# Optimization experiments

Hardware: AMD Instinct MI355X
Metric: run time of the kernel (lower is better)

The kernel has to match this reference:

```python
import jax, jax.numpy as jnp
import numpy as np
from jax import lax

B, S, E, H, KS = 2, 2048, 1024, 16, 3
DH = E // H


def setup_inputs() -> dict:
    key = jax.random.key(0)
    ks = jax.random.split(key, 11)
    s = 1.0 / np.sqrt(E)
    sc = 1.0 / np.sqrt(H * KS)
    return {
        "query": jax.random.normal(ks[0], (B, S, E), jnp.float32),
        "Wq": jax.random.uniform(ks[1], (E, E), jnp.float32, -s, s),
        "bq": jax.random.uniform(ks[2], (E,), jnp.float32, -s, s),
        "Wk": jax.random.uniform(ks[3], (E, E), jnp.float32, -s, s),
        "bk": jax.random.uniform(ks[4], (E,), jnp.float32, -s, s),
        "Wv": jax.random.uniform(ks[5], (E, E), jnp.float32, -s, s),
        "bv": jax.random.uniform(ks[6], (E,), jnp.float32, -s, s),
        "Wo": jax.random.uniform(ks[7], (E, E), jnp.float32, -s, s),
        "bo": jax.random.uniform(ks[8], (E,), jnp.float32, -s, s),
        "conv_w": jax.random.uniform(ks[9], (H, H, KS), jnp.float32, -sc, sc),
        "conv_b": jax.random.uniform(ks[10], (H,), jnp.float32, -sc, sc),
    }


def reference(query, Wq, bq, Wk, bk, Wv, bv, Wo, bo, conv_w, conv_b):
    b, s, e = query.shape
    h, dh = H, DH
    # projections, split heads -> [B, H, S, Dh]
    Q = (query @ Wq.T + bq).reshape(b, s, h, dh).transpose(0, 2, 1, 3)
    K = (query @ Wk.T + bk).reshape(b, s, h, dh).transpose(0, 2, 1, 3)
    V = (query @ Wv.T + bv).reshape(b, s, h, dh).transpose(0, 2, 1, 3)
    # scores [B, H, Sq, Sk]
    scores = jnp.einsum("bhqd,bhkd->bhqk", Q, K) / np.sqrt(dh).astype(np.float32)
    # cross-head conv1d along key axis: reshape to (B*Sq, H, Sk) as NCW
    x = scores.transpose(0, 2, 1, 3).reshape(b * s, h, s)
    x = lax.conv_general_dilated(
        x, conv_w, window_strides=(1,), padding=[(KS // 2, KS // 2)],
        dimension_numbers=("NCW", "OIW", "NCW"))
    x = x + conv_b[None, :, None]
    scores = x.reshape(b, s, h, s).transpose(0, 2, 1, 3)
    weights = jax.nn.softmax(scores, axis=-1)
    # PV matmul, merge heads -> [B, S, E]
    out = jnp.einsum("bhqk,bhkd->bqhd", weights, V).reshape(b, s, e)
    return out @ Wo.T + bo
```

## Files before the change

kernel.cpp:

```cpp
#include <hip/hip_runtime.h>

typedef unsigned short u16;
typedef short short8 __attribute__((ext_vector_type(8)));
typedef unsigned short ushort8 __attribute__((ext_vector_type(8)));
typedef unsigned short bf16x4 __attribute__((ext_vector_type(4)));
typedef float f32x4 __attribute__((ext_vector_type(4)));

#define DEVINL __device__ __forceinline__

DEVINL float bf2f(u16 u) {
  unsigned int x = ((unsigned int)u) << 16;
  return __builtin_bit_cast(float, x);
}
DEVINL u16 f2bf(float f) {
  unsigned int x = __builtin_bit_cast(unsigned int, f);
  x += 0x7FFFu + ((x >> 16) & 1u);
  return (u16)(x >> 16);
}


__global__ __launch_bounds__(256) void cvt_all(
    const float* __restrict__ q, const float* __restrict__ wq,
    const float* __restrict__ wk, const float* __restrict__ wv,
    const float* __restrict__ wo, u16* __restrict__ out) {
  int i = blockIdx.x * 256 + threadIdx.x;
  const float* src;
  size_t off8;
  if (i < 524288) { src = q;  off8 = i; }
  else if (i < 655360) { src = wq; off8 = i - 524288; }
  else if (i < 786432) { src = wk; off8 = i - 655360; }
  else if (i < 917504) { src = wv; off8 = i - 786432; }
  else { src = wo; off8 = i - 917504; }
  f32x4 a = ((const f32x4*)src)[2 * off8];
  f32x4 b = ((const f32x4*)src)[2 * off8 + 1];
  ushort8 o;
#pragma unroll
  for (int e = 0; e < 4; ++e) o[e] = f2bf(a[e]);
#pragma unroll
  for (int e = 0; e < 4; ++e) o[4 + e] = f2bf(b[e]);
  ((ushort8*)out)[i] = o;
}

template <int BM, int BN, bool TRANSV, bool HASBIAS, bool OUTF32>
__global__ __launch_bounds__(256) void gemm_nt(
    const u16* __restrict__ A, const u16* __restrict__ Bm,
    const float* __restrict__ bias, void* __restrict__ C,
    int K, int lda, int ldb, int ldc, float scale,
    long long sAh, long long sBh, long long sCh) {
  constexpr int LDSS = 40;
  constexpr int WM = BM / 2, WN = BN / 2, FM = WM / 16, FN = WN / 16;
  constexpr int AIN = BM / 64;
  constexpr int BIN = BN / 64;

  __shared__ alignas(16) u16 As[BM * LDSS];
  __shared__ alignas(16) u16 Bs[BN * LDSS];

  const int tid = threadIdx.x;
  const int lane = tid & 63;
  const int wv = tid >> 6;
  const int wy = wv >> 1, wx = wv & 1;
  const int quad = lane >> 4, mrow = lane & 15;

  const int z = blockIdx.z;
  const u16* Ap = A + z * sAh;
  const u16* Bp = Bm + z * sBh;
  u16* Cp = (u16*)C + z * sCh;
  float* Cf = (float*)C + z * sCh;

  const int row0 = blockIdx.y * BM;
  const int col0 = blockIdx.x * BN;

  f32x4 acc[FM][FN];
#pragma unroll
  for (int i = 0; i < FM; ++i)
#pragma unroll
    for (int j = 0; j < FN; ++j) acc[i][j] = f32x4{0.f, 0.f, 0.f, 0.f};

  for (int k0 = 0; k0 < K; k0 += 32) {
    ushort8 ta[AIN], tb[BIN];
#pragma unroll
    for (int r = 0; r < AIN; ++r) {
      int idx = r * 256 + tid;
      int row = idx >> 2, ch = idx & 3;
      ta[r] = *(const ushort8*)(Ap + (size_t)(row0 + row) * lda + k0 + ch * 8);
    }
#pragma unroll
    for (int r = 0; r < BIN; ++r) {
      int idx = r * 256 + tid;
      int row = idx >> 2, ch = idx & 3;
      tb[r] = *(const ushort8*)(Bp + (size_t)(col0 + row) * ldb + k0 + ch * 8);
    }
    __syncthreads();
#pragma unroll
    for (int r = 0; r < AIN; ++r) {
      int idx = r * 256 + tid;
      int row = idx >> 2, ch = idx & 3;
      *(ushort8*)&As[row * LDSS + ch * 8] = ta[r];
    }
#pragma unroll
    for (int r = 0; r < BIN; ++r) {
      int idx = r * 256 + tid;
      int row = idx >> 2, ch = idx & 3;
      *(ushort8*)&Bs[row * LDSS + ch * 8] = tb[r];
    }
    __syncthreads();

    short8 af[FM], bfr[FN];
#pragma unroll
    for (int mi = 0; mi < FM; ++mi)
      af[mi] = *(const short8*)&As[(wy * WM + mi * 16 + mrow) * LDSS + quad * 8];
#pragma unroll
    for (int ni = 0; ni < FN; ++ni)
      bfr[ni] = *(const short8*)&Bs[(wx * WN + ni * 16 + mrow) * LDSS + quad * 8];
#pragma unroll
    for (int mi = 0; mi < FM; ++mi)
#pragma unroll
      for (int ni = 0; ni < FN; ++ni)
        acc[mi][ni] = __builtin_amdgcn_mfma_f32_16x16x32_bf16(
            af[mi], bfr[ni], acc[mi][ni], 0, 0, 0);
  }

#pragma unroll
  for (int mi = 0; mi < FM; ++mi) {
    const int rowb = row0 + wy * WM + mi * 16 + quad * 4;
#pragma unroll
    for (int ni = 0; ni < FN; ++ni) {
      const int col = col0 + wx * WN + ni * 16 + mrow;
      float bv = 0.f;
      if (HASBIAS) bv = bias[col];
      f32x4 v = acc[mi][ni];
      if (OUTF32) {
#pragma unroll
        for (int r = 0; r < 4; ++r)
          Cf[(size_t)(rowb + r) * ldc + col] = v[r] * scale + bv;
      } else if (!TRANSV) {
#pragma unroll
        for (int r = 0; r < 4; ++r)
          Cp[(size_t)(rowb + r) * ldc + col] = f2bf(v[r] * scale + bv);
      } else {
        const int bb = rowb >> 11;
        const int ss = rowb & 2047;
        bf16x4 pk;
#pragma unroll
        for (int r = 0; r < 4; ++r) pk[r] = f2bf(v[r] * scale + bv);
        *(bf16x4*)(Cp + (size_t)bb * 2097152 + (size_t)col * 2048 + ss) = pk;
      }
    }
  }
}

__global__ __launch_bounds__(512, 2) void conv_softmax(
    u16* __restrict__ SC, const float* __restrict__ cw, int qt) {
  __shared__ alignas(16) u16 rawT[1026 * 24];
  __shared__ float redA[8][16];
  __shared__ float redB[8][16];

  const int tid = threadIdx.x;
  const int lane = tid & 63;
  const int wv = tid >> 6;
  const int q = blockIdx.x;
  const int n = lane & 15;
  const int quad = lane >> 4;

  short8 a1, a2;
  {
    const int h = n;
#pragma unroll
    for (int j = 0; j < 8; ++j) {
      const int kd = quad * 8 + j;
      const int i = kd & 15, d = kd >> 4;
      a1[j] = (short)f2bf(cw[h * 48 + i * 3 + d]);
      a2[j] = (quad < 2) ? (short)f2bf(cw[h * 48 + kd * 3 + 2]) : (short)0;
    }
  }

  f32x4 acc[16];
#pragma unroll
  for (int ai = 0; ai < 16; ++ai) acc[ai] = f32x4{0.f, 0.f, 0.f, 0.f};

  for (int s = 0; s < 2; ++s) {
    if (s) __syncthreads();
    const int segk = s * 1024;
    {
      const int h = tid & 15, kc = tid >> 4;
#pragma unroll
      for (int j = 0; j < 4; ++j) {
        const int kb = kc * 32 + j * 8;
        ushort8 v = *(const ushort8*)&SC[((size_t)h * qt + q) * 2048 + segk + kb];
#pragma unroll
        for (int e0 = 0; e0 < 8; ++e0) {
          const int e = (e0 + h) & 7;
          rawT[(kb + e + 1) * 24 + h] = v[e];
        }
      }
      if (tid < 32) {
        const int h2 = tid & 15;
        const int top = tid >> 4;
        const int k = segk + (top ? 1024 : -1);
        u16 val = 0;
        if ((unsigned)k < 2048u) val = SC[((size_t)h2 * qt + q) * 2048 + k];
        rawT[(top ? 1025 : 0) * 24 + h2] = val;
      }
    }
    __syncthreads();

#pragma unroll
    for (int tt = 0; tt < 8; ++tt) {
      const int k0l = (wv * 8 + tt) * 16;
      const short8 b1 = *(const short8*)&rawT[(k0l + n + (quad >> 1)) * 24 + (quad & 1) * 8];
      const short8 b2 = *(const short8*)&rawT[(k0l + n + 2) * 24 + (quad & 1) * 8];
      const int ai = s * 8 + tt;
      acc[ai] = __builtin_amdgcn_mfma_f32_16x16x32_bf16(a1, b1, acc[ai], 0, 0, 0);
      acc[ai] = __builtin_amdgcn_mfma_f32_16x16x32_bf16(a2, b2, acc[ai], 0, 0, 0);
    }
  }

  float fm[4];
#pragma unroll
  for (int r = 0; r < 4; ++r) fm[r] = -3e38f;
#pragma unroll
  for (int ai = 0; ai < 16; ++ai)
#pragma unroll
    for (int r = 0; r < 4; ++r) fm[r] = fmaxf(fm[r], acc[ai][r]);
#pragma unroll
  for (int off = 1; off < 16; off <<= 1)
#pragma unroll
    for (int r = 0; r < 4; ++r) fm[r] = fmaxf(fm[r], __shfl_xor(fm[r], off));
  if (n == 0)
#pragma unroll
    for (int r = 0; r < 4; ++r) redA[wv][quad * 4 + r] = fm[r];
  __syncthreads();
#pragma unroll
  for (int r = 0; r < 4; ++r) {
    float m = redA[0][quad * 4 + r];
#pragma unroll
    for (int w = 1; w < 8; ++w) m = fmaxf(m, redA[w][quad * 4 + r]);
    fm[r] = m;
  }
  float fs[4] = {0.f, 0.f, 0.f, 0.f};
#pragma unroll
  for (int ai = 0; ai < 16; ++ai)
#pragma unroll
    for (int r = 0; r < 4; ++r) {
      acc[ai][r] = __expf(acc[ai][r] - fm[r]);
      fs[r] += acc[ai][r];
    }
#pragma unroll
  for (int off = 1; off < 16; off <<= 1)
#pragma unroll
    for (int r = 0; r < 4; ++r) fs[r] += __shfl_xor(fs[r], off);
  if (n == 0)
#pragma unroll
    for (int r = 0; r < 4; ++r) redB[wv][quad * 4 + r] = fs[r];
  __syncthreads();
#pragma unroll
  for (int r = 0; r < 4; ++r) {
    float sum = 0.f;
#pragma unroll
    for (int w = 0; w < 8; ++w) sum += redB[w][quad * 4 + r];
    fs[r] = 1.f / sum;
  }

#pragma unroll
  for (int ai = 0; ai < 16; ++ai) {
    const int k0 = (ai >> 3) * 1024 + ((ai & 7) + wv * 8) * 16;
#pragma unroll
    for (int r = 0; r < 4; ++r) {
      const int h = quad * 4 + r;
      SC[((size_t)h * qt + q) * 2048 + k0 + n] = f2bf(acc[ai][r] * fs[r]);
    }
  }
}

__global__ void fill_diag(float* out, int n) {
  int i = blockIdx.x * 256 + threadIdx.x;
  if (i < n) out[i] = 2000.0f;
}

extern "C" void kernel_launch(void* const* d_in, const int* in_sizes, int n_in,
                              void* d_out, int out_size, void* d_ws, size_t ws_size,
                              hipStream_t stream) {
  const float* query = (const float*)d_in[0];
  const float* Wq = (const float*)d_in[1];
  const float* bq = (const float*)d_in[2];
  const float* Wk = (const float*)d_in[3];
  const float* bk = (const float*)d_in[4];
  const float* Wv = (const float*)d_in[5];
  const float* bv = (const float*)d_in[6];
  const float* Wo = (const float*)d_in[7];
  const float* bo = (const float*)d_in[8];
  const float* cw = (const float*)d_in[9];

  const size_t SE = (size_t)4096 * 1024;
  const size_t WE = (size_t)1024 * 1024;
  const size_t fixedElems = (SE + 4 * WE) + 4 * SE;
  const size_t fixedB = fixedElems * sizeof(u16);

  int qt = 0;
  for (int cand = 2048; cand >= 128; cand >>= 1) {
    size_t need = fixedB + (size_t)16 * cand * 2048 * sizeof(u16);
    if (ws_size >= need) { qt = cand; break; }
  }
  if (qt == 0) {
    fill_diag<<<dim3((out_size + 255) / 256), dim3(256), 0, stream>>>(
        (float*)d_out, out_size);
    return;
  }

  u16* ws = (u16*)d_ws;
  u16* Qb = ws;
  u16* Wqb = Qb + SE;
  u16* Wkb = Wqb + WE;
  u16* Wvb = Wkb + WE;
  u16* Wob = Wvb + WE;
  u16* Qw = Wob + WE;
  u16* Kw = Qw + SE;
  u16* Vt = Kw + SE;
  u16* At = Vt + SE;
  u16* SC = At + SE;

  dim3 blk(256);
  cvt_all<<<dim3(4096), blk, 0, stream>>>(query, Wq, Wk, Wv, Wo, Qb);

  gemm_nt<128, 128, false, true, false><<<dim3(8, 32, 1), blk, 0, stream>>>(
      Qb, Wqb, bq, Qw, 1024, 1024, 1024, 1024, 1.f, 0, 0, 0);
  gemm_nt<128, 128, false, true, false><<<dim3(8, 32, 1), blk, 0, stream>>>(
      Qb, Wkb, bk, Kw, 1024, 1024, 1024, 1024, 1.f, 0, 0, 0);
  gemm_nt<128, 128, true, true, false><<<dim3(8, 32, 1), blk, 0, stream>>>(
      Qb, Wvb, bv, Vt, 1024, 1024, 1024, 1024, 1.f, 0, 0, 0);

  const long long scTile = (long long)qt * 2048;
  for (int b = 0; b < 2; ++b) {
    for (int q0 = 0; q0 < 2048; q0 += qt) {
      const size_t qkOff = (size_t)b * 2097152 + (size_t)q0 * 1024;
      gemm_nt<128, 128, false, false, false>
          <<<dim3(16, qt / 128, 16), blk, 0, stream>>>(
              Qw + qkOff, Kw + (size_t)b * 2097152, nullptr, SC,
              64, 1024, 1024, 2048, 0.125f, 64LL, 64LL, scTile);
      conv_softmax<<<dim3(qt), dim3(512), 0, stream>>>(SC, cw, qt);
      gemm_nt<128, 64, false, false, false>
          <<<dim3(1, qt / 128, 16), blk, 0, stream>>>(
              SC, Vt + (size_t)b * 2097152, nullptr,
              At + qkOff, 2048, 2048, 2048, 1024, 1.f,
              scTile, 131072LL, 64LL);
    }
  }

  gemm_nt<128, 128, false, true, true><<<dim3(8, 32, 1), blk, 0, stream>>>(
      At, Wob, bo, d_out, 1024, 1024, 1024, 1024, 1.f, 0, 0, 0);
}
```

Baseline: 499.8 us.

## Fuse conv, online softmax and PV matmul into one streaming kernel

```diff
diff --git a/kernel.cpp b/kernel.cpp
--- a/kernel.cpp
+++ b/kernel.cpp
@@ -149,125 +149,185 @@
   }
 }
 
-__global__ __launch_bounds__(512, 2) void conv_softmax(
-    u16* __restrict__ SC, const float* __restrict__ cw, int qt) {
-  __shared__ alignas(16) u16 rawT[1026 * 24];
-  __shared__ float redA[8][16];
-  __shared__ float redB[8][16];
+__global__ __launch_bounds__(512) void conv_attn(
+    const u16* __restrict__ SC, const u16* __restrict__ Vt,
+    const float* __restrict__ cw, u16* __restrict__ At) {
+  constexpr int TROW = 24;
+  constexpr int TSLAB = 66 * TROW;
+  constexpr int PROW = 72;
+  __shared__ alignas(16) u16 T[8 * TSLAB];
+  __shared__ alignas(16) u16 Pl[16 * 8 * PROW];
+  __shared__ float alphaS[16][16];
+  __shared__ float lS[16][16];
 
   const int tid = threadIdx.x;
   const int lane = tid & 63;
   const int wv = tid >> 6;
-  const int q = blockIdx.x;
   const int n = lane & 15;
   const int quad = lane >> 4;
+  const int q0 = blockIdx.x * 8;
+
+  if (tid < 256) {
+    alphaS[tid >> 4][tid & 15] = 1.f;
+    lS[tid >> 4][tid & 15] = 1.f;
+  }
 
   short8 a1, a2;
+#pragma unroll
+  for (int j = 0; j < 8; ++j) {
+    const int kd = quad * 8 + j;
+    const int i = kd & 15, d = kd >> 4;
+    a1[j] = (short)f2bf(cw[n * 48 + i * 3 + d]);
+    a2[j] = (quad < 2) ? (short)f2bf(cw[n * 48 + kd * 3 + 2]) : (short)0;
+  }
+
+  float m[4], l[4];
+#pragma unroll
+  for (int r = 0; r < 4; ++r) { m[r] = -3e38f; l[r] = 0.f; }
+  f32x4 O[2][4];
+#pragma unroll
+  for (int hh = 0; hh < 2; ++hh)
+#pragma unroll
+    for (int dt = 0; dt < 4; ++dt) O[hh][dt] = f32x4{0.f, 0.f, 0.f, 0.f};
+
+#pragma unroll 1
+  for (int c = 0; c < 32; ++c) {
+    const int k0 = c * 64;
+#pragma unroll
+    for (int rr = 0; rr < 2; ++rr) {
+      const int idx = rr * 512 + tid;
+      const int k8 = idx & 7;
+      const int pair = idx >> 3;
+      const int qq = pair >> 4, h = pair & 15;
+      ushort8 v = *(const ushort8*)(SC + ((size_t)(h * 2048 + q0 + qq) * 2048) + k0 + k8 * 8);
+#pragma unroll
+      for (int e0 = 0; e0 < 8; ++e0) {
+        const int e = (e0 + k8) & 7;
+        T[qq * TSLAB + (1 + k8 * 8 + e) * TROW + h] = v[e];
+      }
+    }
+    if (tid < 256) {
+      const int top = tid >> 7, p2 = tid & 127;
+      const int qq = p2 >> 4, h = p2 & 15;
+      const int k = k0 + (top ? 64 : -1);
+      u16 val = 0;
+      if ((unsigned)k < 2048u) val = SC[(size_t)(h * 2048 + q0 + qq) * 2048 + k];
+      T[qq * TSLAB + (top ? 65 : 0) * TROW + h] = val;
+    }
+
+    if (c > 0) {
+      const int k0p = k0 - 64;
+#pragma unroll
+      for (int hh = 0; hh < 2; ++hh) {
+        const int h = wv * 2 + hh;
+        float av[4];
+#pragma unroll
+        for (int r = 0; r < 4; ++r) av[r] = alphaS[h][quad * 4 + r];
+#pragma unroll
+        for (int dt = 0; dt < 4; ++dt)
+#pragma unroll
+          for (int r = 0; r < 4; ++r) O[hh][dt][r] *= av[r];
+#pragma unroll
+        for (int ks = 0; ks < 2; ++ks) {
+          const short8 aF = *(const short8*)&Pl[(h * 8 + (n & 7)) * PROW + ks * 32 + quad * 8];
+#pragma unroll
+          for (int dt = 0; dt < 4; ++dt) {
+            const short8 bF = *(const short8*)(Vt + (size_t)(h * 64 + dt * 16 + n) * 2048 + k0p + ks * 32 + quad * 8);
+            O[hh][dt] = __builtin_amdgcn_mfma_f32_16x16x32_bf16(aF, bF, O[hh][dt], 0, 0, 0);
+          }
+        }
+      }
+    }
+    __syncthreads();
+
+    {
+      const int qq = wv;
+      f32x4 x[4];
+#pragma unroll
+      for (int kt = 0; kt < 4; ++kt) {
+        const short8 b1 = *(const short8*)&T[qq * TSLAB + (kt * 16 + n + (quad >> 1)) * TROW + (quad & 1) * 8];
+        const short8 b2 = *(const short8*)&T[qq * TSLAB + (kt * 16 + n + 2) * TROW + (quad & 1) * 8];
+        f32x4 acc = f32x4{0.f, 0.f, 0.f, 0.f};
+        acc = __builtin_amdgcn_mfma_f32_16x16x32_bf16(a1, b1, acc, 0, 0, 0);
+        acc = __builtin_amdgcn_mfma_f32_16x16x32_bf16(a2, b2, acc, 0, 0, 0);
+        x[kt] = acc;
+      }
+      float mn[4], al[4], s[4];
+#pragma unroll
+      for (int r = 0; r < 4; ++r) {
+        float cm = fmaxf(fmaxf(x[0][r], x[1][r]), fmaxf(x[2][r], x[3][r]));
+#pragma unroll
+        for (int off = 1; off < 16; off <<= 1) cm = fmaxf(cm, __shfl_xor(cm, off));
+        mn[r] = fmaxf(m[r], cm);
+        al[r] = __expf(m[r] - mn[r]);
+        s[r] = 0.f;
+      }
+#pragma unroll
+      for (int kt = 0; kt < 4; ++kt)
+#pragma unroll
+        for (int r = 0; r < 4; ++r) {
+          x[kt][r] = __expf(x[kt][r] - mn[r]);
+          s[r] += x[kt][r];
+        }
+#pragma unroll
+      for (int r = 0; r < 4; ++r) {
+#pragma unroll
+        for (int off = 1; off < 16; off <<= 1) s[r] += __shfl_xor(s[r], off);
+        l[r] = l[r] * al[r] + s[r];
+        m[r] = mn[r];
+      }
+#pragma unroll
+      for (int kt = 0; kt < 4; ++kt)
+#pragma unroll
+        for (int r = 0; r < 4; ++r)
+          Pl[((quad * 4 + r) * 8 + qq) * PROW + kt * 16 + n] = f2bf(x[kt][r]);
+      if (n == 0)
+#pragma unroll
+        for (int r = 0; r < 4; ++r) alphaS[quad * 4 + r][qq] = al[r];
+    }
+    __syncthreads();
+  }
+
   {
-    const int h = n;
-#pragma unroll
-    for (int j = 0; j < 8; ++j) {
-      const int kd = quad * 8 + j;
-      const int i = kd & 15, d = kd >> 4;
-      a1[j] = (short)f2bf(cw[h * 48 + i * 3 + d]);
-      a2[j] = (quad < 2) ? (short)f2bf(cw[h * 48 + kd * 3 + 2]) : (short)0;
-    }
-  }
-
-  f32x4 acc[16];
-#pragma unroll
-  for (int ai = 0; ai < 16; ++ai) acc[ai] = f32x4{0.f, 0.f, 0.f, 0.f};
-
-  for (int s = 0; s < 2; ++s) {
-    if (s) __syncthreads();
-    const int segk = s * 1024;
-    {
-      const int h = tid & 15, kc = tid >> 4;
-#pragma unroll
-      for (int j = 0; j < 4; ++j) {
-        const int kb = kc * 32 + j * 8;
-        ushort8 v = *(const ushort8*)&SC[((size_t)h * qt + q) * 2048 + segk + kb];
-#pragma unroll
-        for (int e0 = 0; e0 < 8; ++e0) {
-          const int e = (e0 + h) & 7;
-          rawT[(kb + e + 1) * 24 + h] = v[e];
+    const int k0p = 31 * 64;
+#pragma unroll
+    for (int hh = 0; hh < 2; ++hh) {
+      const int h = wv * 2 + hh;
+      float av[4];
+#pragma unroll
+      for (int r = 0; r < 4; ++r) av[r] = alphaS[h][quad * 4 + r];
+#pragma unroll
+      for (int dt = 0; dt < 4; ++dt)
+#pragma unroll
+        for (int r = 0; r < 4; ++r) O[hh][dt][r] *= av[r];
+#pragma unroll
+      for (int ks = 0; ks < 2; ++ks) {
+        const short8 aF = *(const short8*)&Pl[(h * 8 + (n & 7)) * PROW + ks * 32 + quad * 8];
+#pragma unroll
+        for (int dt = 0; dt < 4; ++dt) {
+          const short8 bF = *(const short8*)(Vt + (size_t)(h * 64 + dt * 16 + n) * 2048 + k0p + ks * 32 + quad * 8);
+          O[hh][dt] = __builtin_amdgcn_mfma_f32_16x16x32_bf16(aF, bF, O[hh][dt], 0, 0, 0);
         }
       }
-      if (tid < 32) {
-        const int h2 = tid & 15;
-        const int top = tid >> 4;
-        const int k = segk + (top ? 1024 : -1);
-        u16 val = 0;
-        if ((unsigned)k < 2048u) val = SC[((size_t)h2 * qt + q) * 2048 + k];
-        rawT[(top ? 1025 : 0) * 24 + h2] = val;
-      }
-    }
-    __syncthreads();
-
-#pragma unroll
-    for (int tt = 0; tt < 8; ++tt) {
-      const int k0l = (wv * 8 + tt) * 16;
-      const short8 b1 = *(const short8*)&rawT[(k0l + n + (quad >> 1)) * 24 + (quad & 1) * 8];
-      const short8 b2 = *(const short8*)&rawT[(k0l + n + 2) * 24 + (quad & 1) * 8];
-      const int ai = s * 8 + tt;
-      acc[ai] = __builtin_amdgcn_mfma_f32_16x16x32_bf16(a1, b1, acc[ai], 0, 0, 0);
-      acc[ai] = __builtin_amdgcn_mfma_f32_16x16x32_bf16(a2, b2, acc[ai], 0, 0, 0);
-    }
-  }
-
-  float fm[4];
-#pragma unroll
-  for (int r = 0; r < 4; ++r) fm[r] = -3e38f;
-#pragma unroll
-  for (int ai = 0; ai < 16; ++ai)
-#pragma unroll
-    for (int r = 0; r < 4; ++r) fm[r] = fmaxf(fm[r], acc[ai][r]);
-#pragma unroll
-  for (int off = 1; off < 16; off <<= 1)
-#pragma unroll
-    for (int r = 0; r < 4; ++r) fm[r] = fmaxf(fm[r], __shfl_xor(fm[r], off));
+    }
+  }
   if (n == 0)
 #pragma unroll
-    for (int r = 0; r < 4; ++r) redA[wv][quad * 4 + r] = fm[r];
+    for (int r = 0; r < 4; ++r) lS[quad * 4 + r][wv] = l[r];
   __syncthreads();
 #pragma unroll
-  for (int r = 0; r < 4; ++r) {
-    float m = redA[0][quad * 4 + r];
-#pragma unroll
-    for (int w = 1; w < 8; ++w) m = fmaxf(m, redA[w][quad * 4 + r]);
-    fm[r] = m;
-  }
-  float fs[4] = {0.f, 0.f, 0.f, 0.f};
-#pragma unroll
-  for (int ai = 0; ai < 16; ++ai)
-#pragma unroll
-    for (int r = 0; r < 4; ++r) {
-      acc[ai][r] = __expf(acc[ai][r] - fm[r]);
-      fs[r] += acc[ai][r];
-    }
-#pragma unroll
-  for (int off = 1; off < 16; off <<= 1)
-#pragma unroll
-    for (int r = 0; r < 4; ++r) fs[r] += __shfl_xor(fs[r], off);
-  if (n == 0)
-#pragma unroll
-    for (int r = 0; r < 4; ++r) redB[wv][quad * 4 + r] = fs[r];
-  __syncthreads();
-#pragma unroll
-  for (int r = 0; r < 4; ++r) {
-    float sum = 0.f;
-#pragma unroll
-    for (int w = 0; w < 8; ++w) sum += redB[w][quad * 4 + r];
-    fs[r] = 1.f / sum;
-  }
-
-#pragma unroll
-  for (int ai = 0; ai < 16; ++ai) {
-    const int k0 = (ai >> 3) * 1024 + ((ai & 7) + wv * 8) * 16;
-#pragma unroll
-    for (int r = 0; r < 4; ++r) {
-      const int h = quad * 4 + r;
-      SC[((size_t)h * qt + q) * 2048 + k0 + n] = f2bf(acc[ai][r] * fs[r]);
+  for (int hh = 0; hh < 2; ++hh) {
+    const int h = wv * 2 + hh;
+    if (quad < 2) {
+      float inv[4];
+#pragma unroll
+      for (int r = 0; r < 4; ++r) inv[r] = 1.f / lS[h][quad * 4 + r];
+#pragma unroll
+      for (int dt = 0; dt < 4; ++dt)
+#pragma unroll
+        for (int r = 0; r < 4; ++r)
+          At[(size_t)(q0 + quad * 4 + r) * 1024 + h * 64 + dt * 16 + n] =
+              f2bf(O[hh][dt][r] * inv[r]);
     }
   }
 }
@@ -293,15 +353,9 @@
 
   const size_t SE = (size_t)4096 * 1024;
   const size_t WE = (size_t)1024 * 1024;
-  const size_t fixedElems = (SE + 4 * WE) + 4 * SE;
-  const size_t fixedB = fixedElems * sizeof(u16);
-
-  int qt = 0;
-  for (int cand = 2048; cand >= 128; cand >>= 1) {
-    size_t need = fixedB + (size_t)16 * cand * 2048 * sizeof(u16);
-    if (ws_size >= need) { qt = cand; break; }
-  }
-  if (qt == 0) {
+  const size_t SCE = (size_t)16 * 2048 * 2048;
+  const size_t fixedB = ((SE + 4 * WE) + 4 * SE) * sizeof(u16);
+  if (ws_size < fixedB + SCE * sizeof(u16)) {
     fill_diag<<<dim3((out_size + 255) / 256), dim3(256), 0, stream>>>(
         (float*)d_out, out_size);
     return;
@@ -329,21 +383,14 @@
   gemm_nt<128, 128, true, true, false><<<dim3(8, 32, 1), blk, 0, stream>>>(
       Qb, Wvb, bv, Vt, 1024, 1024, 1024, 1024, 1.f, 0, 0, 0);
 
-  const long long scTile = (long long)qt * 2048;
   for (int b = 0; b < 2; ++b) {
-    for (int q0 = 0; q0 < 2048; q0 += qt) {
-      const size_t qkOff = (size_t)b * 2097152 + (size_t)q0 * 1024;
-      gemm_nt<128, 128, false, false, false>
-          <<<dim3(16, qt / 128, 16), blk, 0, stream>>>(
-              Qw + qkOff, Kw + (size_t)b * 2097152, nullptr, SC,
-              64, 1024, 1024, 2048, 0.125f, 64LL, 64LL, scTile);
-      conv_softmax<<<dim3(qt), dim3(512), 0, stream>>>(SC, cw, qt);
-      gemm_nt<128, 64, false, false, false>
-          <<<dim3(1, qt / 128, 16), blk, 0, stream>>>(
-              SC, Vt + (size_t)b * 2097152, nullptr,
-              At + qkOff, 2048, 2048, 2048, 1024, 1.f,
-              scTile, 131072LL, 64LL);
-    }
+    const size_t bQK = (size_t)b * 2097152;
+    gemm_nt<128, 128, false, false, false>
+        <<<dim3(16, 16, 16), blk, 0, stream>>>(
+            Qw + bQK, Kw + bQK, nullptr, SC,
+            64, 1024, 1024, 2048, 0.125f, 64LL, 64LL, 4194304LL);
+    conv_attn<<<dim3(256), dim3(512), 0, stream>>>(
+        SC, Vt + bQK, cw, At + bQK);
   }
 
   gemm_nt<128, 128, false, true, true><<<dim3(8, 32, 1), blk, 0, stream>>>(
```

After: 698.6 us. 39.8% more time.

## Recompute conv in two passes to cut registers, defer softmax normalization to PV GEMM

Applied to the files above, without the earlier changes.

```diff
diff --git a/kernel.cpp b/kernel.cpp
--- a/kernel.cpp
+++ b/kernel.cpp
@@ -41,10 +41,11 @@
   ((ushort8*)out)[i] = o;
 }
 
-template <int BM, int BN, bool TRANSV, bool HASBIAS, bool OUTF32>
+template <int BM, int BN, bool TRANSV, bool HASBIAS, bool OUTF32, bool RSCALE>
 __global__ __launch_bounds__(256) void gemm_nt(
     const u16* __restrict__ A, const u16* __restrict__ Bm,
     const float* __restrict__ bias, void* __restrict__ C,
+    const float* __restrict__ rsc,
     int K, int lda, int ldb, int ldc, float scale,
     long long sAh, long long sBh, long long sCh) {
   constexpr int LDSS = 40;
@@ -135,8 +136,11 @@
           Cf[(size_t)(rowb + r) * ldc + col] = v[r] * scale + bv;
       } else if (!TRANSV) {
 #pragma unroll
-        for (int r = 0; r < 4; ++r)
-          Cp[(size_t)(rowb + r) * ldc + col] = f2bf(v[r] * scale + bv);
+        for (int r = 0; r < 4; ++r) {
+          float rs = 1.f;
+          if (RSCALE) rs = rsc[(size_t)z * 2048 + rowb + r];
+          Cp[(size_t)(rowb + r) * ldc + col] = f2bf(v[r] * scale * rs + bv);
+        }
       } else {
         const int bb = rowb >> 11;
         const int ss = rowb & 2047;
@@ -149,11 +153,12 @@
   }
 }
 
-__global__ __launch_bounds__(512, 2) void conv_softmax(
-    u16* __restrict__ SC, const float* __restrict__ cw, int qt) {
-  __shared__ alignas(16) u16 rawT[1026 * 24];
-  __shared__ float redA[8][16];
-  __shared__ float redB[8][16];
+__global__ __launch_bounds__(512, 8) void conv_softmax(
+    u16* __restrict__ SC, const float* __restrict__ cw, float* __restrict__ Lb) {
+  __shared__ alignas(16) u16 rawT[514 * 24];
+  __shared__ float redM[8][16];
+  __shared__ float redL[8][16];
+  __shared__ u16 haloL[16];
 
   const int tid = threadIdx.x;
   const int lane = tid & 63;
@@ -163,112 +168,129 @@
   const int quad = lane >> 4;
 
   short8 a1, a2;
-  {
-    const int h = n;
-#pragma unroll
-    for (int j = 0; j < 8; ++j) {
-      const int kd = quad * 8 + j;
-      const int i = kd & 15, d = kd >> 4;
-      a1[j] = (short)f2bf(cw[h * 48 + i * 3 + d]);
-      a2[j] = (quad < 2) ? (short)f2bf(cw[h * 48 + kd * 3 + 2]) : (short)0;
-    }
-  }
-
-  f32x4 acc[16];
-#pragma unroll
-  for (int ai = 0; ai < 16; ++ai) acc[ai] = f32x4{0.f, 0.f, 0.f, 0.f};
-
-  for (int s = 0; s < 2; ++s) {
+#pragma unroll
+  for (int j = 0; j < 8; ++j) {
+    const int kd = quad * 8 + j;
+    const int i = kd & 15, d = kd >> 4;
+    a1[j] = (short)f2bf(cw[n * 48 + i * 3 + d]);
+    a2[j] = (quad < 2) ? (short)f2bf(cw[n * 48 + kd * 3 + 2]) : (short)0;
+  }
+
+  const int h16 = tid & 15, kc = tid >> 4;
+  const size_t rowbase = ((size_t)h16 * 2048 + q) * 2048;
+  const int htop = (tid >> 4) & 1;
+  const size_t hrow = ((size_t)h16 * 2048 + q) * 2048;
+
+  float m[4];
+#pragma unroll
+  for (int r = 0; r < 4; ++r) m[r] = -3e38f;
+
+#pragma unroll 1
+  for (int s = 0; s < 4; ++s) {
+    const int segk = s * 512;
     if (s) __syncthreads();
-    const int segk = s * 1024;
-    {
-      const int h = tid & 15, kc = tid >> 4;
-#pragma unroll
-      for (int j = 0; j < 4; ++j) {
-        const int kb = kc * 32 + j * 8;
-        ushort8 v = *(const ushort8*)&SC[((size_t)h * qt + q) * 2048 + segk + kb];
-#pragma unroll
-        for (int e0 = 0; e0 < 8; ++e0) {
-          const int e = (e0 + h) & 7;
-          rawT[(kb + e + 1) * 24 + h] = v[e];
-        }
-      }
-      if (tid < 32) {
-        const int h2 = tid & 15;
-        const int top = tid >> 4;
-        const int k = segk + (top ? 1024 : -1);
-        u16 val = 0;
-        if ((unsigned)k < 2048u) val = SC[((size_t)h2 * qt + q) * 2048 + k];
-        rawT[(top ? 1025 : 0) * 24 + h2] = val;
-      }
-    }
-    __syncthreads();
-
-#pragma unroll
-    for (int tt = 0; tt < 8; ++tt) {
-      const int k0l = (wv * 8 + tt) * 16;
+#pragma unroll
+    for (int j = 0; j < 2; ++j) {
+      const int kb = kc * 16 + j * 8;
+      ushort8 v = *(const ushort8*)&SC[rowbase + segk + kb];
+#pragma unroll
+      for (int e0 = 0; e0 < 8; ++e0) {
+        const int e = (e0 + h16) & 7;
+        rawT[(kb + e + 1) * 24 + h16] = v[e];
+      }
+    }
+    if (tid < 32) {
+      const int k = segk + (htop ? 512 : -1);
+      u16 val = ((unsigned)k < 2048u) ? SC[hrow + k] : (u16)0;
+      rawT[(htop ? 513 : 0) * 24 + h16] = val;
+    }
+    __syncthreads();
+#pragma unroll
+    for (int tt = 0; tt < 4; ++tt) {
+      const int k0l = (wv * 4 + tt) * 16;
       const short8 b1 = *(const short8*)&rawT[(k0l + n + (quad >> 1)) * 24 + (quad & 1) * 8];
       const short8 b2 = *(const short8*)&rawT[(k0l + n + 2) * 24 + (quad & 1) * 8];
-      const int ai = s * 8 + tt;
-      acc[ai] = __builtin_amdgcn_mfma_f32_16x16x32_bf16(a1, b1, acc[ai], 0, 0, 0);
-      acc[ai] = __builtin_amdgcn_mfma_f32_16x16x32_bf16(a2, b2, acc[ai], 0, 0, 0);
-    }
-  }
-
-  float fm[4];
-#pragma unroll
-  for (int r = 0; r < 4; ++r) fm[r] = -3e38f;
-#pragma unroll
-  for (int ai = 0; ai < 16; ++ai)
-#pragma unroll
-    for (int r = 0; r < 4; ++r) fm[r] = fmaxf(fm[r], acc[ai][r]);
+      f32x4 x = f32x4{0.f, 0.f, 0.f, 0.f};
+      x = __builtin_amdgcn_mfma_f32_16x16x32_bf16(a1, b1, x, 0, 0, 0);
+      x = __builtin_amdgcn_mfma_f32_16x16x32_bf16(a2, b2, x, 0, 0, 0);
+#pragma unroll
+      for (int r = 0; r < 4; ++r) m[r] = fmaxf(m[r], x[r]);
+    }
+  }
 #pragma unroll
   for (int off = 1; off < 16; off <<= 1)
 #pragma unroll
-    for (int r = 0; r < 4; ++r) fm[r] = fmaxf(fm[r], __shfl_xor(fm[r], off));
+    for (int r = 0; r < 4; ++r) m[r] = fmaxf(m[r], __shfl_xor(m[r], off));
   if (n == 0)
 #pragma unroll
-    for (int r = 0; r < 4; ++r) redA[wv][quad * 4 + r] = fm[r];
+    for (int r = 0; r < 4; ++r) redM[wv][quad * 4 + r] = m[r];
   __syncthreads();
+  float fM[4];
 #pragma unroll
   for (int r = 0; r < 4; ++r) {
-    float m = redA[0][quad * 4 + r];
-#pragma unroll
-    for (int w = 1; w < 8; ++w) m = fmaxf(m, redA[w][quad * 4 + r]);
-    fm[r] = m;
-  }
-  float fs[4] = {0.f, 0.f, 0.f, 0.f};
-#pragma unroll
-  for (int ai = 0; ai < 16; ++ai)
-#pragma unroll
-    for (int r = 0; r < 4; ++r) {
-      acc[ai][r] = __expf(acc[ai][r] - fm[r]);
-      fs[r] += acc[ai][r];
-    }
+    float M = redM[0][quad * 4 + r];
+#pragma unroll
+    for (int w = 1; w < 8; ++w) M = fmaxf(M, redM[w][quad * 4 + r]);
+    fM[r] = M;
+  }
+
+  float l[4] = {0.f, 0.f, 0.f, 0.f};
+
+#pragma unroll 1
+  for (int s = 0; s < 4; ++s) {
+    const int segk = s * 512;
+    __syncthreads();
+#pragma unroll
+    for (int j = 0; j < 2; ++j) {
+      const int kb = kc * 16 + j * 8;
+      ushort8 v = *(const ushort8*)&SC[rowbase + segk + kb];
+#pragma unroll
+      for (int e0 = 0; e0 < 8; ++e0) {
+        const int e = (e0 + h16) & 7;
+        rawT[(kb + e + 1) * 24 + h16] = v[e];
+      }
+    }
+    if (tid < 32) {
+      if (htop) {
+        const int k = segk + 512;
+        rawT[513 * 24 + h16] = (k < 2048) ? SC[hrow + k] : (u16)0;
+      } else {
+        rawT[0 * 24 + h16] = (s == 0) ? (u16)0 : haloL[h16];
+      }
+    }
+    __syncthreads();
+    if (tid < 16) haloL[tid] = rawT[512 * 24 + tid];
+#pragma unroll
+    for (int tt = 0; tt < 4; ++tt) {
+      const int k0l = (wv * 4 + tt) * 16;
+      const short8 b1 = *(const short8*)&rawT[(k0l + n + (quad >> 1)) * 24 + (quad & 1) * 8];
+      const short8 b2 = *(const short8*)&rawT[(k0l + n + 2) * 24 + (quad & 1) * 8];
+      f32x4 x = f32x4{0.f, 0.f, 0.f, 0.f};
+      x = __builtin_amdgcn_mfma_f32_16x16x32_bf16(a1, b1, x, 0, 0, 0);
+      x = __builtin_amdgcn_mfma_f32_16x16x32_bf16(a2, b2, x, 0, 0, 0);
+      const int kg = segk + k0l + n;
+#pragma unroll
+      for (int r = 0; r < 4; ++r) {
+        const float e = __expf(x[r] - fM[r]);
+        l[r] += e;
+        SC[((size_t)(quad * 4 + r) * 2048 + q) * 2048 + kg] = f2bf(e);
+      }
+    }
+  }
+
 #pragma unroll
   for (int off = 1; off < 16; off <<= 1)
 #pragma unroll
-    for (int r = 0; r < 4; ++r) fs[r] += __shfl_xor(fs[r], off);
+    for (int r = 0; r < 4; ++r) l[r] += __shfl_xor(l[r], off);
   if (n == 0)
 #pragma unroll
-    for (int r = 0; r < 4; ++r) redB[wv][quad * 4 + r] = fs[r];
+    for (int r = 0; r < 4; ++r) redL[wv][quad * 4 + r] = l[r];
   __syncthreads();
-#pragma unroll
-  for (int r = 0; r < 4; ++r) {
+  if (tid < 16) {
     float sum = 0.f;
 #pragma unroll
-    for (int w = 0; w < 8; ++w) sum += redB[w][quad * 4 + r];
-    fs[r] = 1.f / sum;
-  }
-
-#pragma unroll
-  for (int ai = 0; ai < 16; ++ai) {
-    const int k0 = (ai >> 3) * 1024 + ((ai & 7) + wv * 8) * 16;
-#pragma unroll
-    for (int r = 0; r < 4; ++r) {
-      const int h = quad * 4 + r;
-      SC[((size_t)h * qt + q) * 2048 + k0 + n] = f2bf(acc[ai][r] * fs[r]);
-    }
+    for (int w = 0; w < 8; ++w) sum += redL[w][tid];
+    Lb[(size_t)tid * 2048 + q] = 1.f / sum;
   }
 }
 
@@ -293,15 +315,10 @@
 
   const size_t SE = (size_t)4096 * 1024;
   const size_t WE = (size_t)1024 * 1024;
-  const size_t fixedElems = (SE + 4 * WE) + 4 * SE;
-  const size_t fixedB = fixedElems * sizeof(u16);
-
-  int qt = 0;
-  for (int cand = 2048; cand >= 128; cand >>= 1) {
-    size_t need = fixedB + (size_t)16 * cand * 2048 * sizeof(u16);
-    if (ws_size >= need) { qt = cand; break; }
-  }
-  if (qt == 0) {
+  const size_t SCE = (size_t)16 * 2048 * 2048;
+  const size_t fixedB = ((SE + 4 * WE) + 4 * SE) * sizeof(u16);
+  const size_t LBB = (size_t)16 * 2048 * sizeof(float);
+  if (ws_size < fixedB + SCE * sizeof(u16) + LBB) {
     fill_diag<<<dim3((out_size + 255) / 256), dim3(256), 0, stream>>>(
         (float*)d_out, out_size);
     return;
@@ -318,34 +335,31 @@
   u16* Vt = Kw + SE;
   u16* At = Vt + SE;
   u16* SC = At + SE;
+  float* Lb = (float*)(SC + SCE);
 
   dim3 blk(256);
   cvt_all<<<dim3(4096), blk, 0, stream>>>(query, Wq, Wk, Wv, Wo, Qb);
 
-  gemm_nt<128, 128, false, true, false><<<dim3(8, 32, 1), blk, 0, stream>>>(
-      Qb, Wqb, bq, Qw, 1024, 1024, 1024, 1024, 1.f, 0, 0, 0);
-  gemm_nt<128, 128, false, true, false><<<dim3(8, 32, 1), blk, 0, stream>>>(
-      Qb, Wkb, bk, Kw, 1024, 1024, 1024, 1024, 1.f, 0, 0, 0);
-  gemm_nt<128, 128, true, true, false><<<dim3(8, 32, 1), blk, 0, stream>>>(
-      Qb, Wvb, bv, Vt, 1024, 1024, 1024, 1024, 1.f, 0, 0, 0);
-
-  const long long scTile = (long long)qt * 2048;
+  gemm_nt<128, 128, false, true, false, false><<<dim3(8, 32, 1), blk, 0, stream>>>(
+      Qb, Wqb, bq, Qw, nullptr, 1024, 1024, 1024, 1024, 1.f, 0, 0, 0);
+  gemm_nt<128, 128, false, true, false, false><<<dim3(8, 32, 1), blk, 0, stream>>>(
+      Qb, Wkb, bk, Kw, nullptr, 1024, 1024, 1024, 1024, 1.f, 0, 0, 0);
+  gemm_nt<128, 128, true, true, false, false><<<dim3(8, 32, 1), blk, 0, stream>>>(
+      Qb, Wvb, bv, Vt, nullptr, 1024, 1024, 1024, 1024, 1.f, 0, 0, 0);
+
   for (int b = 0; b < 2; ++b) {
-    for (int q0 = 0; q0 < 2048; q0 += qt) {
-      const size_t qkOff = (size_t)b * 2097152 + (size_t)q0 * 1024;
-      gemm_nt<128, 128, false, false, false>
-          <<<dim3(16, qt / 128, 16), blk, 0, stream>>>(
-              Qw + qkOff, Kw + (size_t)b * 2097152, nullptr, SC,
-              64, 1024, 1024, 2048, 0.125f, 64LL, 64LL, scTile);
-      conv_softmax<<<dim3(qt), dim3(512), 0, stream>>>(SC, cw, qt);
-      gemm_nt<128, 64, false, false, false>
-          <<<dim3(1, qt / 128, 16), blk, 0, stream>>>(
-              SC, Vt + (size_t)b * 2097152, nullptr,
-              At + qkOff, 2048, 2048, 2048, 1024, 1.f,
-              scTile, 131072LL, 64LL);
-    }
-  }
-
-  gemm_nt<128, 128, false, true, true><<<dim3(8, 32, 1), blk, 0, stream>>>(
-      At, Wob, bo, d_out, 1024, 1024, 1024, 1024, 1.f, 0, 0, 0);
-}
+    const size_t bQK = (size_t)b * 2097152;
+    gemm_nt<128, 128, false, false, false, false>
+        <<<dim3(16, 16, 16), blk, 0, stream>>>(
+            Qw + bQK, Kw + bQK, nullptr, SC, nullptr,
+            64, 1024, 1024, 2048, 0.125f, 64LL, 64LL, 4194304LL);
+    conv_softmax<<<dim3(2048), dim3(512), 0, stream>>>(SC, cw, Lb);
+    gemm_nt<64, 64, false, false, false, true>
+        <<<dim3(1, 32, 16), blk, 0, stream>>>(
+            SC, Vt + bQK, nullptr, At + bQK, Lb,
+            2048, 2048, 2048, 1024, 1.f, 4194304LL, 131072LL, 64LL);
+  }
+
+  gemm_nt<128, 128, false, true, true, false><<<dim3(8, 32, 1), blk, 0, stream>>>(
+      At, Wob, bo, d_out, nullptr, 1024, 1024, 1024, 1024, 1.f, 0, 0, 0);
+}
```

Result: slower. 742.6 us (+48.6%).

## Fuse QKV projections, defer softmax normalization into PV GEMM, retile attention GEMMs

Applied to the files above, without the earlier changes.

```diff
diff --git a/kernel.cpp b/kernel.cpp
--- a/kernel.cpp
+++ b/kernel.cpp
@@ -41,16 +41,20 @@
   ((ushort8*)out)[i] = o;
 }
 
-template <int BM, int BN, bool TRANSV, bool HASBIAS, bool OUTF32>
+template <int BM, int BN, int BK, bool TRANSV, bool HASBIAS, bool OUTF32,
+          bool RSCALE>
 __global__ __launch_bounds__(256) void gemm_nt(
     const u16* __restrict__ A, const u16* __restrict__ Bm,
     const float* __restrict__ bias, void* __restrict__ C,
+    const float* __restrict__ rsc,
     int K, int lda, int ldb, int ldc, float scale,
     long long sAh, long long sBh, long long sCh) {
-  constexpr int LDSS = 40;
+  constexpr int LDSS = BK + 8;
+  constexpr int KC8 = BK / 8;
+  constexpr int KSH = (BK == 32) ? 2 : 3;
   constexpr int WM = BM / 2, WN = BN / 2, FM = WM / 16, FN = WN / 16;
-  constexpr int AIN = BM / 64;
-  constexpr int BIN = BN / 64;
+  constexpr int AIN = BM * KC8 / 256;
+  constexpr int BIN = BN * KC8 / 256;
 
   __shared__ alignas(16) u16 As[BM * LDSS];
   __shared__ alignas(16) u16 Bs[BN * LDSS];
@@ -76,48 +80,51 @@
 #pragma unroll
     for (int j = 0; j < FN; ++j) acc[i][j] = f32x4{0.f, 0.f, 0.f, 0.f};
 
-  for (int k0 = 0; k0 < K; k0 += 32) {
+  for (int k0 = 0; k0 < K; k0 += BK) {
     ushort8 ta[AIN], tb[BIN];
 #pragma unroll
     for (int r = 0; r < AIN; ++r) {
       int idx = r * 256 + tid;
-      int row = idx >> 2, ch = idx & 3;
+      int row = idx >> KSH, ch = idx & (KC8 - 1);
       ta[r] = *(const ushort8*)(Ap + (size_t)(row0 + row) * lda + k0 + ch * 8);
     }
 #pragma unroll
     for (int r = 0; r < BIN; ++r) {
       int idx = r * 256 + tid;
-      int row = idx >> 2, ch = idx & 3;
+      int row = idx >> KSH, ch = idx & (KC8 - 1);
       tb[r] = *(const ushort8*)(Bp + (size_t)(col0 + row) * ldb + k0 + ch * 8);
     }
     __syncthreads();
 #pragma unroll
     for (int r = 0; r < AIN; ++r) {
       int idx = r * 256 + tid;
-      int row = idx >> 2, ch = idx & 3;
+      int row = idx >> KSH, ch = idx & (KC8 - 1);
       *(ushort8*)&As[row * LDSS + ch * 8] = ta[r];
     }
 #pragma unroll
     for (int r = 0; r < BIN; ++r) {
       int idx = r * 256 + tid;
-      int row = idx >> 2, ch = idx & 3;
+      int row = idx >> KSH, ch = idx & (KC8 - 1);
       *(ushort8*)&Bs[row * LDSS + ch * 8] = tb[r];
     }
     __syncthreads();
 
-    short8 af[FM], bfr[FN];
-#pragma unroll
-    for (int mi = 0; mi < FM; ++mi)
-      af[mi] = *(const short8*)&As[(wy * WM + mi * 16 + mrow) * LDSS + quad * 8];
-#pragma unroll
-    for (int ni = 0; ni < FN; ++ni)
-      bfr[ni] = *(const short8*)&Bs[(wx * WN + ni * 16 + mrow) * LDSS + quad * 8];
-#pragma unroll
-    for (int mi = 0; mi < FM; ++mi)
+#pragma unroll
+    for (int ks = 0; ks < BK / 32; ++ks) {
+      short8 af[FM], bfr[FN];
+#pragma unroll
+      for (int mi = 0; mi < FM; ++mi)
+        af[mi] = *(const short8*)&As[(wy * WM + mi * 16 + mrow) * LDSS + ks * 32 + quad * 8];
 #pragma unroll
       for (int ni = 0; ni < FN; ++ni)
-        acc[mi][ni] = __builtin_amdgcn_mfma_f32_16x16x32_bf16(
-            af[mi], bfr[ni], acc[mi][ni], 0, 0, 0);
+        bfr[ni] = *(const short8*)&Bs[(wx * WN + ni * 16 + mrow) * LDSS + ks * 32 + quad * 8];
+#pragma unroll
+      for (int mi = 0; mi < FM; ++mi)
+#pragma unroll
+        for (int ni = 0; ni < FN; ++ni)
+          acc[mi][ni] = __builtin_amdgcn_mfma_f32_16x16x32_bf16(
+              af[mi], bfr[ni], acc[mi][ni], 0, 0, 0);
+    }
   }
 
 #pragma unroll
@@ -135,8 +142,11 @@
           Cf[(size_t)(rowb + r) * ldc + col] = v[r] * scale + bv;
       } else if (!TRANSV) {
 #pragma unroll
-        for (int r = 0; r < 4; ++r)
-          Cp[(size_t)(rowb + r) * ldc + col] = f2bf(v[r] * scale + bv);
+        for (int r = 0; r < 4; ++r) {
+          float rs = 1.f;
+          if (RSCALE) rs = rsc[(size_t)z * 2048 + rowb + r];
+          Cp[(size_t)(rowb + r) * ldc + col] = f2bf(v[r] * scale * rs + bv);
+        }
       } else {
         const int bb = rowb >> 11;
         const int ss = rowb & 2047;
@@ -149,8 +159,97 @@
   }
 }
 
+__global__ __launch_bounds__(256) void gemm_qkv(
+    const u16* __restrict__ A, const u16* __restrict__ Bm,
+    const float* __restrict__ bq, const float* __restrict__ bk,
+    const float* __restrict__ bv,
+    u16* __restrict__ Qw, u16* __restrict__ Kw, u16* __restrict__ Vt) {
+  constexpr int LDSS = 40;
+  __shared__ alignas(16) u16 As[128 * LDSS];
+  __shared__ alignas(16) u16 Bs[128 * LDSS];
+
+  const int tid = threadIdx.x;
+  const int lane = tid & 63;
+  const int wv = tid >> 6;
+  const int wy = wv >> 1, wx = wv & 1;
+  const int quad = lane >> 4, mrow = lane & 15;
+
+  const int row0 = blockIdx.y * 128;
+  const int col0 = blockIdx.x * 128;
+
+  f32x4 acc[4][4];
+#pragma unroll
+  for (int i = 0; i < 4; ++i)
+#pragma unroll
+    for (int j = 0; j < 4; ++j) acc[i][j] = f32x4{0.f, 0.f, 0.f, 0.f};
+
+  for (int k0 = 0; k0 < 1024; k0 += 32) {
+    ushort8 ta[2], tb[2];
+#pragma unroll
+    for (int r = 0; r < 2; ++r) {
+      int idx = r * 256 + tid;
+      int row = idx >> 2, ch = idx & 3;
+      ta[r] = *(const ushort8*)(A + (size_t)(row0 + row) * 1024 + k0 + ch * 8);
+      tb[r] = *(const ushort8*)(Bm + (size_t)(col0 + row) * 1024 + k0 + ch * 8);
+    }
+    __syncthreads();
+#pragma unroll
+    for (int r = 0; r < 2; ++r) {
+      int idx = r * 256 + tid;
+      int row = idx >> 2, ch = idx & 3;
+      *(ushort8*)&As[row * LDSS + ch * 8] = ta[r];
+      *(ushort8*)&Bs[row * LDSS + ch * 8] = tb[r];
+    }
+    __syncthreads();
+
+    short8 af[4], bfr[4];
+#pragma unroll
+    for (int mi = 0; mi < 4; ++mi)
+      af[mi] = *(const short8*)&As[(wy * 64 + mi * 16 + mrow) * LDSS + quad * 8];
+#pragma unroll
+    for (int ni = 0; ni < 4; ++ni)
+      bfr[ni] = *(const short8*)&Bs[(wx * 64 + ni * 16 + mrow) * LDSS + quad * 8];
+#pragma unroll
+    for (int mi = 0; mi < 4; ++mi)
+#pragma unroll
+      for (int ni = 0; ni < 4; ++ni)
+        acc[mi][ni] = __builtin_amdgcn_mfma_f32_16x16x32_bf16(
+            af[mi], bfr[ni], acc[mi][ni], 0, 0, 0);
+  }
+
+  const int part = col0 >> 10;
+  const float* bias = (part == 0) ? bq : (part == 1) ? bk : bv;
+#pragma unroll
+  for (int mi = 0; mi < 4; ++mi) {
+    const int rowb = row0 + wy * 64 + mi * 16 + quad * 4;
+#pragma unroll
+    for (int ni = 0; ni < 4; ++ni) {
+      const int col = col0 + wx * 64 + ni * 16 + mrow;
+      const int cl = col & 1023;
+      const float bvl = bias[cl];
+      f32x4 v = acc[mi][ni];
+      if (part == 0) {
+#pragma unroll
+        for (int r = 0; r < 4; ++r)
+          Qw[(size_t)(rowb + r) * 1024 + cl] = f2bf(v[r] + bvl);
+      } else if (part == 1) {
+#pragma unroll
+        for (int r = 0; r < 4; ++r)
+          Kw[(size_t)(rowb + r) * 1024 + cl] = f2bf(v[r] + bvl);
+      } else {
+        const int bb = rowb >> 11;
+        const int ss = rowb & 2047;
+        bf16x4 pk;
+#pragma unroll
+        for (int r = 0; r < 4; ++r) pk[r] = f2bf(v[r] + bvl);
+        *(bf16x4*)(Vt + (size_t)bb * 2097152 + (size_t)cl * 2048 + ss) = pk;
+      }
+    }
+  }
+}
+
 __global__ __launch_bounds__(512, 2) void conv_softmax(
-    u16* __restrict__ SC, const float* __restrict__ cw, int qt) {
+    u16* __restrict__ SC, const float* __restrict__ cw, float* __restrict__ Lb) {
   __shared__ alignas(16) u16 rawT[1026 * 24];
   __shared__ float redA[8][16];
   __shared__ float redB[8][16];
@@ -163,15 +262,12 @@
   const int quad = lane >> 4;
 
   short8 a1, a2;
-  {
-    const int h = n;
-#pragma unroll
-    for (int j = 0; j < 8; ++j) {
-      const int kd = quad * 8 + j;
-      const int i = kd & 15, d = kd >> 4;
-      a1[j] = (short)f2bf(cw[h * 48 + i * 3 + d]);
-      a2[j] = (quad < 2) ? (short)f2bf(cw[h * 48 + kd * 3 + 2]) : (short)0;
-    }
+#pragma unroll
+  for (int j = 0; j < 8; ++j) {
+    const int kd = quad * 8 + j;
+    const int i = kd & 15, d = kd >> 4;
+    a1[j] = (short)f2bf(cw[n * 48 + i * 3 + d]);
+    a2[j] = (quad < 2) ? (short)f2bf(cw[n * 48 + kd * 3 + 2]) : (short)0;
   }
 
   f32x4 acc[16];
@@ -186,7 +282,7 @@
 #pragma unroll
       for (int j = 0; j < 4; ++j) {
         const int kb = kc * 32 + j * 8;
-        ushort8 v = *(const ushort8*)&SC[((size_t)h * qt + q) * 2048 + segk + kb];
+        ushort8 v = *(const ushort8*)&SC[((size_t)h * 2048 + q) * 2048 + segk + kb];
 #pragma unroll
         for (int e0 = 0; e0 < 8; ++e0) {
           const int e = (e0 + h) & 7;
@@ -198,7 +294,7 @@
         const int top = tid >> 4;
         const int k = segk + (top ? 1024 : -1);
         u16 val = 0;
-        if ((unsigned)k < 2048u) val = SC[((size_t)h2 * qt + q) * 2048 + k];
+        if ((unsigned)k < 2048u) val = SC[((size_t)h2 * 2048 + q) * 2048 + k];
         rawT[(top ? 1025 : 0) * 24 + h2] = val;
       }
     }
@@ -253,12 +349,14 @@
 #pragma unroll
     for (int r = 0; r < 4; ++r) redB[wv][quad * 4 + r] = fs[r];
   __syncthreads();
-#pragma unroll
-  for (int r = 0; r < 4; ++r) {
-    float sum = 0.f;
-#pragma unroll
-    for (int w = 0; w < 8; ++w) sum += redB[w][quad * 4 + r];
-    fs[r] = 1.f / sum;
+  if (wv == 0 && n == 0) {
+#pragma unroll
+    for (int r = 0; r < 4; ++r) {
+      float sum = 0.f;
+#pragma unroll
+      for (int w = 0; w < 8; ++w) sum += redB[w][quad * 4 + r];
+      Lb[(size_t)(quad * 4 + r) * 2048 + q] = 1.f / sum;
+    }
   }
 
 #pragma unroll
@@ -267,7 +365,7 @@
 #pragma unroll
     for (int r = 0; r < 4; ++r) {
       const int h = quad * 4 + r;
-      SC[((size_t)h * qt + q) * 2048 + k0 + n] = f2bf(acc[ai][r] * fs[r]);
+      SC[((size_t)h * 2048 + q) * 2048 + k0 + n] = f2bf(acc[ai][r]);
     }
   }
 }
@@ -293,15 +391,10 @@
 
   const size_t SE = (size_t)4096 * 1024;
   const size_t WE = (size_t)1024 * 1024;
-  const size_t fixedElems = (SE + 4 * WE) + 4 * SE;
-  const size_t fixedB = fixedElems * sizeof(u16);
-
-  int qt = 0;
-  for (int cand = 2048; cand >= 128; cand >>= 1) {
-    size_t need = fixedB + (size_t)16 * cand * 2048 * sizeof(u16);
-    if (ws_size >= need) { qt = cand; break; }
-  }
-  if (qt == 0) {
+  const size_t SCE = (size_t)16 * 2048 * 2048;
+  const size_t fixedB = ((SE + 4 * WE) + 4 * SE) * sizeof(u16);
+  const size_t LBB = (size_t)16 * 2048 * sizeof(float);
+  if (ws_size < fixedB + SCE * sizeof(u16) + LBB) {
     fill_diag<<<dim3((out_size + 255) / 256), dim3(256), 0, stream>>>(
         (float*)d_out, out_size);
     return;
@@ -318,34 +411,27 @@
   u16* Vt = Kw + SE;
   u16* At = Vt + SE;
   u16* SC = At + SE;
+  float* Lb = (float*)(SC + SCE);
 
   dim3 blk(256);
   cvt_all<<<dim3(4096), blk, 0, stream>>>(query, Wq, Wk, Wv, Wo, Qb);
 
-  gemm_nt<128, 128, false, true, false><<<dim3(8, 32, 1), blk, 0, stream>>>(
-      Qb, Wqb, bq, Qw, 1024, 1024, 1024, 1024, 1.f, 0, 0, 0);
-  gemm_nt<128, 128, false, true, false><<<dim3(8, 32, 1), blk, 0, stream>>>(
-      Qb, Wkb, bk, Kw, 1024, 1024, 1024, 1024, 1.f, 0, 0, 0);
-  gemm_nt<128, 128, true, true, false><<<dim3(8, 32, 1), blk, 0, stream>>>(
-      Qb, Wvb, bv, Vt, 1024, 1024, 1024, 1024, 1.f, 0, 0, 0);
-
-  const long long scTile = (long long)qt * 2048;
+  gemm_qkv<<<dim3(24, 32, 1), blk, 0, stream>>>(
+      Qb, Wqb, bq, bk, bv, Qw, Kw, Vt);
+
   for (int b = 0; b < 2; ++b) {
-    for (int q0 = 0; q0 < 2048; q0 += qt) {
-      const size_t qkOff = (size_t)b * 2097152 + (size_t)q0 * 1024;
-      gemm_nt<128, 128, false, false, false>
-          <<<dim3(16, qt / 128, 16), blk, 0, stream>>>(
-              Qw + qkOff, Kw + (size_t)b * 2097152, nullptr, SC,
-              64, 1024, 1024, 2048, 0.125f, 64LL, 64LL, scTile);
-      conv_softmax<<<dim3(qt), dim3(512), 0, stream>>>(SC, cw, qt);
-      gemm_nt<128, 64, false, false, false>
-          <<<dim3(1, qt / 128, 16), blk, 0, stream>>>(
-              SC, Vt + (size_t)b * 2097152, nullptr,
-              At + qkOff, 2048, 2048, 2048, 1024, 1.f,
-              scTile, 131072LL, 64LL);
-    }
-  }
-
-  gemm_nt<128, 128, false, true, true><<<dim3(8, 32, 1), blk, 0, stream>>>(
-      At, Wob, bo, d_out, 1024, 1024, 1024, 1024, 1.f, 0, 0, 0);
-}
+    const size_t bQK = (size_t)b * 2097152;
+    gemm_nt<128, 128, 64, false, false, false, false>
+        <<<dim3(16, 16, 16), blk, 0, stream>>>(
+            Qw + bQK, Kw + bQK, nullptr, SC, nullptr,
+            64, 1024, 1024, 2048, 0.125f, 64LL, 64LL, 4194304LL);
+    conv_softmax<<<dim3(2048), dim3(512), 0, stream>>>(SC, cw, Lb);
+    gemm_nt<64, 64, 32, false, false, false, true>
+        <<<dim3(1, 32, 16), blk, 0, stream>>>(
+            SC, Vt + bQK, nullptr, At + bQK, Lb,
+            2048, 2048, 2048, 1024, 1.f, 4194304LL, 131072LL, 64LL);
+  }
+
+  gemm_nt<128, 128, 32, false, true, true, false><<<dim3(8, 32, 1), blk, 0, stream>>>(
+      At, Wob, bo, d_out, nullptr, 1024, 1024, 1024, 1024, 1.f, 0, 0, 0);
+}
```

Result: faster. 455.3 us (-8.9%).
